# Performance work log

Measured on AMD Instinct MI355X. Metric: run time of the kernel, lower is better.

The kernel has to match this reference:

```python
import jax, jax.numpy as jnp
import numpy as np

MAX_ITER = 20
F_TOL = 1e-6
FREE_NUM = 64  # free_idx[1] + 1
TRUNC = (0, 512)  # truncate_idx


def setup_inputs() -> dict:
    key = jax.random.key(0)
    ks = jax.random.split(key, 8)
    bsz, in_dim, hid, out_dim, m = 1024, 512, 1024, 256, 128
    return {
        "b_primal": jax.random.normal(ks[0], (bsz, in_dim), jnp.float32),
        "W0": jax.random.normal(ks[1], (hid, in_dim), jnp.float32) / np.sqrt(in_dim).astype(np.float32),
        "b0": jnp.zeros((hid,), jnp.float32),
        "W1": jax.random.normal(ks[2], (hid, hid), jnp.float32) / np.sqrt(hid).astype(np.float32),
        "b1": jnp.zeros((hid,), jnp.float32),
        "W2": jax.random.normal(ks[3], (out_dim, hid), jnp.float32) / np.sqrt(hid).astype(np.float32),
        "b2": jnp.zeros((out_dim,), jnp.float32),
        "A": jax.random.normal(ks[4], (m, out_dim), jnp.float32) * 0.1,
        "b_vec": jax.random.normal(ks[5], (m,), jnp.float32),
        # scaled so spectral norm < 1 -> contracting fixed-point iteration
        "WzProj": jax.random.normal(ks[6], (out_dim, out_dim), jnp.float32) * 0.03,
        "WbProj": jax.random.normal(ks[7], (out_dim, m), jnp.float32) * 0.1,
    }


def reference(b_primal, W0, b0, W1, b1, W2, b2, A, b_vec, WzProj, WbProj):
    # eval-mode forward of DualNN (report_projection=True)
    x = b_primal[:, TRUNC[0]:TRUNC[1]]
    h = jax.nn.relu(x @ W0.T + b0)
    h = jax.nn.relu(h @ W1.T + b1)
    out = h @ W2.T + b2                      # [bsz, output_dim]

    bias_proj = b_vec @ WbProj.T             # [output_dim]

    def cond(state):
        _, it, res = state
        return (it <= MAX_ITER) & (res > F_TOL)

    def body(state):
        z, it, _ = state
        z = bias_proj + z @ WzProj.T         # affine projection step
        u = z[:, :FREE_NUM]
        v = jax.nn.relu(z[:, FREE_NUM:])     # clamp non-free coordinates
        z = jnp.concatenate([u, v], axis=-1)
        res = jnp.max(jnp.abs(z @ A.T - b_vec))  # inf-norm equality residual
        return z, it + 1, res

    z_star, curr_iter, _ = jax.lax.while_loop(
        cond, body, (out, jnp.int32(1), jnp.float32(jnp.inf)))
    return (z_star, out, curr_iter)
```

## Files before the change

kernel.cpp:

```cpp
#include <hip/hip_runtime.h>

typedef __attribute__((ext_vector_type(8))) __bf16 bf16x8;
typedef __attribute__((ext_vector_type(4))) float f32x4;

#define MAX_ITER_N 20
#define F_TOL_F 1e-6f
#define FREE_NUM_N 64

#define BSZ 1024
#define IN_DIM 512
#define HID 1024
#define OUT_DIM 256
#define M_CON 128

#define WS_BP    0
#define WS_RES   256
#define WS_CTRL  288
#define WS_H1    296
#define WS_H2    (WS_H1 + 524288)
#define WS_APC   (WS_H2 + 524288)
#define WS_W0C   (WS_APC + 262144)
#define WS_W1C   (WS_W0C + 262144)
#define WS_W2C   (WS_W1C + 524288)
#define WS_WZG   (WS_W2C + 131072)
#define WS_AG    (WS_WZG + 32768)

__device__ __forceinline__ unsigned short f2bf(float f) {
    unsigned int u = __float_as_uint(f);
    u += 0x7fffu + ((u >> 16) & 1u);
    return (unsigned short)(u >> 16);
}

__device__ __forceinline__ void gload_lds16(const unsigned short* g, unsigned short* l) {
    __builtin_amdgcn_global_load_lds(
        (const __attribute__((address_space(1))) unsigned int*)(const void*)g,
        (__attribute__((address_space(3))) unsigned int*)(void*)l, 16, 0, 0);
}

__global__ __launch_bounds__(256) void prep_k(
    const float* __restrict__ b_primal, const float* __restrict__ W0,
    const float* __restrict__ W1, const float* __restrict__ W2,
    const float* __restrict__ Wz, const float* __restrict__ Am,
    const float* __restrict__ b_vec, const float* __restrict__ WbProj,
    unsigned short* __restrict__ APc, unsigned short* __restrict__ W0c,
    unsigned short* __restrict__ W1c, unsigned short* __restrict__ W2c,
    unsigned short* __restrict__ WzG, unsigned short* __restrict__ AG,
    float* __restrict__ bp, unsigned int* __restrict__ res)
{
    int b = blockIdx.x;
    if (b >= 2400) {
        int j = threadIdx.x;
        float s = 0.0f;
        for (int k = 0; k < M_CON; ++k) s += b_vec[k] * WbProj[j * M_CON + k];
        bp[j] = s;
        if (j < 32) res[j] = 0u;
        return;
    }
    const float* src; unsigned short* dst; int off;
    if (b < 512)       { src = b_primal; dst = APc; off = b; }
    else if (b < 1024) { src = W0; dst = W0c; off = b - 512; }
    else if (b < 2048) { src = W1; dst = W1c; off = b - 1024; }
    else if (b < 2304) { src = W2; dst = W2c; off = b - 2048; }
    else if (b < 2368) { src = Wz; dst = WzG; off = b - 2304; }
    else               { src = Am; dst = AG;  off = b - 2368; }
    int idx = off * 1024 + threadIdx.x * 4;
    float4 v = *(const float4*)(src + idx);
    ushort4 o;
    o.x = f2bf(v.x); o.y = f2bf(v.y); o.z = f2bf(v.z); o.w = f2bf(v.w);
    *(ushort4*)(dst + idx) = o;
}

__device__ __forceinline__ void stage_tile(const unsigned short* __restrict__ src,
                                           unsigned short* lds, int ldK, int w, int lane) {
#pragma unroll
    for (int i = 0; i < 2; ++i) {
        int gbase = i * 256 + w * 64;
        int g = gbase + lane;
        int row = g >> 3;
        int sgc = (g & 7) ^ (row & 7);
        gload_lds16(src + row * ldK + sgc * 8, lds + gbase * 8);
    }
}

__device__ __forceinline__ bf16x8 frag_ld(const unsigned short* lds, int row, int j) {
    int phys = j ^ (row & 7);
    return __builtin_bit_cast(bf16x8, *(const uint4*)(lds + row * 64 + phys * 8));
}

template<int K, bool RELU, bool F32OUT>
__global__ __launch_bounds__(256) void mfma_gemm(
    const unsigned short* __restrict__ A,
    const unsigned short* __restrict__ B,
    const float* __restrict__ bias,
    void* __restrict__ Cv, int N_)
{
    __shared__ __align__(16) unsigned short As[64 * 64];
    __shared__ __align__(16) unsigned short Bs[64 * 64];
    const int tid = threadIdx.x;
    const int w = tid >> 6;
    const int lane = tid & 63;
    const int ln = lane & 15;
    const int q  = lane >> 4;
    const int row0 = blockIdx.y * 64;
    const int col0 = blockIdx.x * 64;

    const unsigned short* Ab = A + row0 * K;
    const unsigned short* Bb = B + col0 * K;

    f32x4 acc[2][2];
#pragma unroll
    for (int rt = 0; rt < 2; ++rt)
#pragma unroll
        for (int ct = 0; ct < 2; ++ct)
            acc[rt][ct] = (f32x4){0.f, 0.f, 0.f, 0.f};

    for (int k0 = 0; k0 < K; k0 += 64) {
        stage_tile(Ab + k0, As, K, w, lane);
        stage_tile(Bb + k0, Bs, K, w, lane);
        __syncthreads();
#pragma unroll
        for (int ks = 0; ks < 2; ++ks) {
            bf16x8 af[2], bfv[2];
#pragma unroll
            for (int rt = 0; rt < 2; ++rt)
                af[rt] = frag_ld(As, (w >> 1) * 32 + rt * 16 + ln, ks * 4 + q);
#pragma unroll
            for (int ct = 0; ct < 2; ++ct)
                bfv[ct] = frag_ld(Bs, (w & 1) * 32 + ct * 16 + ln, ks * 4 + q);
#pragma unroll
            for (int rt = 0; rt < 2; ++rt)
#pragma unroll
                for (int ct = 0; ct < 2; ++ct)
                    acc[rt][ct] = __builtin_amdgcn_mfma_f32_16x16x32_bf16(
                        af[rt], bfv[ct], acc[rt][ct], 0, 0, 0);
        }
        __syncthreads();
    }

    float bv[2];
#pragma unroll
    for (int ct = 0; ct < 2; ++ct)
        bv[ct] = bias[col0 + (w & 1) * 32 + ct * 16 + ln];
#pragma unroll
    for (int rt = 0; rt < 2; ++rt)
#pragma unroll
        for (int ct = 0; ct < 2; ++ct) {
            int c = col0 + (w & 1) * 32 + ct * 16 + ln;
#pragma unroll
            for (int i = 0; i < 4; ++i) {
                int r = row0 + (w >> 1) * 32 + rt * 16 + q * 4 + i;
                float v = acc[rt][ct][i] + bv[ct];
                if (RELU) v = fmaxf(v, 0.0f);
                if (F32OUT) ((float*)Cv)[r * N_ + c] = v;
                else ((unsigned short*)Cv)[r * N_ + c] = f2bf(v);
            }
        }
}

__global__ __launch_bounds__(256, 1) void loop_fused_k(
    const float* __restrict__ z0,
    const unsigned short* __restrict__ WzG,
    const unsigned short* __restrict__ AG,
    const float* __restrict__ bp,
    const float* __restrict__ b_vec,
    float* __restrict__ zout_g,
    unsigned int* __restrict__ res)
{
    __shared__ unsigned short zS[16][264];
    __shared__ float red[4];

    const int tid  = threadIdx.x;
    const int wave = tid >> 6;
    const int lane = tid & 63;
    const int ln   = lane & 15;
    const int q    = lane >> 4;
    const int r0   = blockIdx.x * 16;

    {
        int row = tid >> 4;
        int c0  = (tid & 15) * 16;
        const float* src = z0 + (r0 + row) * OUT_DIM + c0;
#pragma unroll
        for (int i = 0; i < 16; ++i) zS[row][c0 + i] = f2bf(src[i]);
    }

    bf16x8 afr[2][8];
    float bvv[2];
#pragma unroll
    for (int mt = 0; mt < 2; ++mt) {
        int m = wave * 32 + mt * 16 + ln;
        bvv[mt] = b_vec[m];
#pragma unroll
        for (int ks = 0; ks < 8; ++ks)
            afr[mt][ks] = __builtin_bit_cast(bf16x8, *(const uint4*)(AG + m * OUT_DIM + ks * 32 + q * 8));
    }
    int colg[4];
    float bpv[4];
    bf16x8 wzfr[4][8];
#pragma unroll
    for (int nt = 0; nt < 4; ++nt) {
        colg[nt] = wave * 64 + nt * 16 + ln;
        bpv[nt]  = bp[colg[nt]];
#pragma unroll
        for (int ks = 0; ks < 8; ++ks)
            wzfr[nt][ks] = __builtin_bit_cast(bf16x8, *(const uint4*)(WzG + colg[nt] * OUT_DIM + ks * 32 + q * 8));
    }

    __syncthreads();

    bf16x8 zfr[8];
#pragma unroll
    for (int ks = 0; ks < 8; ++ks)
        zfr[ks] = __builtin_bit_cast(bf16x8, *(const uint4*)&zS[ln][ks * 32 + q * 8]);

    const f32x4 zero4 = {0.f, 0.f, 0.f, 0.f};

    for (int t = 1; t <= MAX_ITER_N; ++t) {
        f32x4 acc[4];
#pragma unroll
        for (int nt = 0; nt < 4; ++nt) acc[nt] = zero4;
#pragma unroll
        for (int ks = 0; ks < 8; ++ks)
#pragma unroll
            for (int nt = 0; nt < 4; ++nt)
                acc[nt] = __builtin_amdgcn_mfma_f32_16x16x32_bf16(zfr[ks], wzfr[nt][ks], acc[nt], 0, 0, 0);
        float vals[4][4];
#pragma unroll
        for (int nt = 0; nt < 4; ++nt)
#pragma unroll
            for (int i = 0; i < 4; ++i) {
                float v = acc[nt][i] + bpv[nt];
                if (colg[nt] >= FREE_NUM_N) v = fmaxf(v, 0.0f);
                vals[nt][i] = v;
            }
        if (t == MAX_ITER_N) {
#pragma unroll
            for (int nt = 0; nt < 4; ++nt)
#pragma unroll
                for (int i = 0; i < 4; ++i)
                    zout_g[(r0 + q * 4 + i) * OUT_DIM + colg[nt]] = vals[nt][i];
        }
        __syncthreads();
#pragma unroll
        for (int nt = 0; nt < 4; ++nt)
#pragma unroll
            for (int i = 0; i < 4; ++i)
                zS[q * 4 + i][colg[nt]] = f2bf(vals[nt][i]);
        __syncthreads();
#pragma unroll
        for (int ks = 0; ks < 8; ++ks)
            zfr[ks] = __builtin_bit_cast(bf16x8, *(const uint4*)&zS[ln][ks * 32 + q * 8]);

        f32x4 acc2[2];
        acc2[0] = zero4; acc2[1] = zero4;
#pragma unroll
        for (int ks = 0; ks < 8; ++ks)
#pragma unroll
            for (int mt = 0; mt < 2; ++mt)
                acc2[mt] = __builtin_amdgcn_mfma_f32_16x16x32_bf16(zfr[ks], afr[mt][ks], acc2[mt], 0, 0, 0);
        float lmax = 0.0f;
#pragma unroll
        for (int mt = 0; mt < 2; ++mt)
#pragma unroll
            for (int i = 0; i < 4; ++i)
                lmax = fmaxf(lmax, fabsf(acc2[mt][i] - bvv[mt]));
#pragma unroll
        for (int off = 32; off > 0; off >>= 1)
            lmax = fmaxf(lmax, __shfl_xor(lmax, off));
        if (lane == 0) red[wave] = lmax;
        __syncthreads();
        if (tid == 0) {
            float bm = fmaxf(fmaxf(red[0], red[1]), fmaxf(red[2], red[3]));
            atomicMax(res + (t - 1), __float_as_uint(bm));
        }
    }
}

__global__ void decide_k(const unsigned int* __restrict__ res, int* __restrict__ ctrl,
                         float* __restrict__ out) {
    int T = MAX_ITER_N;
    for (int t = 0; t < MAX_ITER_N; ++t) {
        float r = __uint_as_float(res[t]);
        if (!(r > F_TOL_F)) { T = t + 1; break; }
    }
    ctrl[0] = T;
    out[2 * BSZ * OUT_DIM] = (float)(T + 1);
}

__global__ __launch_bounds__(256) void fallback_k(
    const float* __restrict__ z0, const float* __restrict__ Wz,
    const float* __restrict__ bp, const int* __restrict__ ctrl,
    float* __restrict__ out)
{
    const int T = ctrl[0];
    if (T >= MAX_ITER_N) return;
    __shared__ float zS[16][257];
    const int r0 = blockIdx.x * 16;
    const int tid = threadIdx.x;
    const int row = tid >> 4;
    const int c0 = (tid & 15) * 16;
    for (int i = 0; i < 16; ++i) zS[row][c0 + i] = z0[(r0 + row) * OUT_DIM + c0 + i];
    __syncthreads();
    const int j = tid;
    const float bj = bp[j];
    for (int t = 0; t < T; ++t) {
        float acc[16] = {};
        for (int k = 0; k < OUT_DIM; ++k) {
            float w = Wz[j * OUT_DIM + k];
#pragma unroll
            for (int r = 0; r < 16; ++r) acc[r] += zS[r][k] * w;
        }
        __syncthreads();
#pragma unroll
        for (int r = 0; r < 16; ++r) {
            float v = acc[r] + bj;
            if (j >= FREE_NUM_N) v = fmaxf(v, 0.0f);
            zS[r][j] = v;
        }
        __syncthreads();
    }
    for (int i = 0; i < 16; ++i) out[(r0 + row) * OUT_DIM + c0 + i] = zS[row][c0 + i];
}

extern "C" void kernel_launch(void* const* d_in, const int* in_sizes, int n_in,
                              void* d_out, int out_size, void* d_ws, size_t ws_size,
                              hipStream_t stream) {
    const float* b_primal = (const float*)d_in[0];
    const float* W0     = (const float*)d_in[1];
    const float* b0     = (const float*)d_in[2];
    const float* W1     = (const float*)d_in[3];
    const float* b1     = (const float*)d_in[4];
    const float* W2     = (const float*)d_in[5];
    const float* b2     = (const float*)d_in[6];
    const float* Amat   = (const float*)d_in[7];
    const float* b_vec  = (const float*)d_in[8];
    const float* WzProj = (const float*)d_in[9];
    const float* WbProj = (const float*)d_in[10];
    float* out = (float*)d_out;
    float* ws  = (float*)d_ws;

    float* bp = ws + WS_BP;
    unsigned int* res = (unsigned int*)(ws + WS_RES);
    int* ctrl = (int*)(ws + WS_CTRL);
    unsigned short* h1c = (unsigned short*)(ws + WS_H1);
    unsigned short* h2c = (unsigned short*)(ws + WS_H2);
    unsigned short* APc = (unsigned short*)(ws + WS_APC);
    unsigned short* W0c = (unsigned short*)(ws + WS_W0C);
    unsigned short* W1c = (unsigned short*)(ws + WS_W1C);
    unsigned short* W2c = (unsigned short*)(ws + WS_W2C);
    unsigned short* WzG = (unsigned short*)(ws + WS_WZG);
    unsigned short* AG  = (unsigned short*)(ws + WS_AG);

    float* outz = out + BSZ * OUT_DIM;

    hipLaunchKernelGGL(prep_k, dim3(2401), dim3(256), 0, stream,
                       b_primal, W0, W1, W2, WzProj, Amat, b_vec, WbProj,
                       APc, W0c, W1c, W2c, WzG, AG, bp, res);

    hipLaunchKernelGGL((mfma_gemm<IN_DIM, true, false>), dim3(HID / 64, BSZ / 64), dim3(256),
                       0, stream, APc, W0c, b0, (void*)h1c, HID);
    hipLaunchKernelGGL((mfma_gemm<HID, true, false>), dim3(HID / 64, BSZ / 64), dim3(256),
                       0, stream, h1c, W1c, b1, (void*)h2c, HID);
    hipLaunchKernelGGL((mfma_gemm<HID, false, true>), dim3(OUT_DIM / 64, BSZ / 64), dim3(256),
                       0, stream, h2c, W2c, b2, (void*)outz, OUT_DIM);

    hipLaunchKernelGGL(loop_fused_k, dim3(BSZ / 16), dim3(256), 0, stream,
                       outz, WzG, AG, bp, b_vec, out, res);
    hipLaunchKernelGGL(decide_k, dim3(1), dim3(1), 0, stream, res, ctrl, out);
    hipLaunchKernelGGL(fallback_k, dim3(BSZ / 16), dim3(256), 0, stream,
                       outz, WzProj, bp, ctrl, out);
}
```

Before: 148.1 us.

## Fuse all stages into one persistent kernel with software grid barriers

Replaces the seven-kernel pipeline (prep, three GEMMs, fixed-point loop, decide, fallback) with a single persistent kernel of 256 blocks that separates phases with an atomic-counter grid barrier. A memset clears the barrier and residual slots before launch. The goal is to remove launch gaps and inter-kernel tail effects. In exchange, each GEMM is capped at one tile per block with 256 blocks and launch_bounds(256,1), the loop phase uses only 64 blocks, and correctness relies on all 256 blocks being co-resident.

```diff
diff --git a/kernel.cpp b/kernel.cpp
--- a/kernel.cpp
+++ b/kernel.cpp
@@ -12,11 +12,12 @@
 #define HID 1024
 #define OUT_DIM 256
 #define M_CON 128
-
-#define WS_BP    0
-#define WS_RES   256
-#define WS_CTRL  288
-#define WS_H1    296
+#define NBLK 256
+
+#define WS_BAR   0
+#define WS_RES   8
+#define WS_BP    48
+#define WS_H1    304
 #define WS_H2    (WS_H1 + 524288)
 #define WS_APC   (WS_H2 + 524288)
 #define WS_W0C   (WS_APC + 262144)
@@ -37,37 +38,20 @@
         (__attribute__((address_space(3))) unsigned int*)(void*)l, 16, 0, 0);
 }
 
-__global__ __launch_bounds__(256) void prep_k(
-    const float* __restrict__ b_primal, const float* __restrict__ W0,
-    const float* __restrict__ W1, const float* __restrict__ W2,
-    const float* __restrict__ Wz, const float* __restrict__ Am,
-    const float* __restrict__ b_vec, const float* __restrict__ WbProj,
-    unsigned short* __restrict__ APc, unsigned short* __restrict__ W0c,
-    unsigned short* __restrict__ W1c, unsigned short* __restrict__ W2c,
-    unsigned short* __restrict__ WzG, unsigned short* __restrict__ AG,
-    float* __restrict__ bp, unsigned int* __restrict__ res)
-{
-    int b = blockIdx.x;
-    if (b >= 2400) {
-        int j = threadIdx.x;
-        float s = 0.0f;
-        for (int k = 0; k < M_CON; ++k) s += b_vec[k] * WbProj[j * M_CON + k];
-        bp[j] = s;
-        if (j < 32) res[j] = 0u;
-        return;
-    }
-    const float* src; unsigned short* dst; int off;
-    if (b < 512)       { src = b_primal; dst = APc; off = b; }
-    else if (b < 1024) { src = W0; dst = W0c; off = b - 512; }
-    else if (b < 2048) { src = W1; dst = W1c; off = b - 1024; }
-    else if (b < 2304) { src = W2; dst = W2c; off = b - 2048; }
-    else if (b < 2368) { src = Wz; dst = WzG; off = b - 2304; }
-    else               { src = Am; dst = AG;  off = b - 2368; }
-    int idx = off * 1024 + threadIdx.x * 4;
-    float4 v = *(const float4*)(src + idx);
-    ushort4 o;
-    o.x = f2bf(v.x); o.y = f2bf(v.y); o.z = f2bf(v.z); o.w = f2bf(v.w);
-    *(ushort4*)(dst + idx) = o;
+__device__ __forceinline__ void grid_barrier(unsigned int* bar) {
+    __syncthreads();
+    if (threadIdx.x == 0) {
+        unsigned int g = __hip_atomic_load(&bar[1], __ATOMIC_RELAXED, __HIP_MEMORY_SCOPE_AGENT);
+        unsigned int a = __hip_atomic_fetch_add(&bar[0], 1u, __ATOMIC_ACQ_REL, __HIP_MEMORY_SCOPE_AGENT);
+        if (a == (unsigned int)(NBLK - 1)) {
+            __hip_atomic_store(&bar[0], 0u, __ATOMIC_RELAXED, __HIP_MEMORY_SCOPE_AGENT);
+            __hip_atomic_store(&bar[1], g + 1u, __ATOMIC_RELEASE, __HIP_MEMORY_SCOPE_AGENT);
+        } else {
+            while (__hip_atomic_load(&bar[1], __ATOMIC_ACQUIRE, __HIP_MEMORY_SCOPE_AGENT) == g)
+                __builtin_amdgcn_s_sleep(2);
+        }
+    }
+    __syncthreads();
 }
 
 __device__ __forceinline__ void stage_tile(const unsigned short* __restrict__ src,
@@ -87,23 +71,22 @@
     return __builtin_bit_cast(bf16x8, *(const uint4*)(lds + row * 64 + phys * 8));
 }
 
-template<int K, bool RELU, bool F32OUT>
-__global__ __launch_bounds__(256) void mfma_gemm(
-    const unsigned short* __restrict__ A,
-    const unsigned short* __restrict__ B,
-    const float* __restrict__ bias,
-    void* __restrict__ Cv, int N_)
+template<bool RELU, bool F32OUT>
+__device__ void gemm_dev(const unsigned short* __restrict__ A,
+                         const unsigned short* __restrict__ B,
+                         const float* __restrict__ bias, void* __restrict__ Cv,
+                         int N_, int K, int tilesN, int ntiles,
+                         unsigned short* As, unsigned short* Bs)
 {
-    __shared__ __align__(16) unsigned short As[64 * 64];
-    __shared__ __align__(16) unsigned short Bs[64 * 64];
+    const int tile = blockIdx.x;
+    if (tile >= ntiles) return;
     const int tid = threadIdx.x;
     const int w = tid >> 6;
     const int lane = tid & 63;
     const int ln = lane & 15;
     const int q  = lane >> 4;
-    const int row0 = blockIdx.y * 64;
-    const int col0 = blockIdx.x * 64;
-
+    const int row0 = (tile / tilesN) * 64;
+    const int col0 = (tile % tilesN) * 64;
     const unsigned short* Ab = A + row0 * K;
     const unsigned short* Bb = B + col0 * K;
 
@@ -157,169 +140,208 @@
         }
 }
 
-__global__ __launch_bounds__(256, 1) void loop_fused_k(
-    const float* __restrict__ z0,
-    const unsigned short* __restrict__ WzG,
-    const unsigned short* __restrict__ AG,
-    const float* __restrict__ bp,
-    const float* __restrict__ b_vec,
-    float* __restrict__ zout_g,
-    unsigned int* __restrict__ res)
+__global__ __launch_bounds__(256, 1) void mega_k(
+    const float* __restrict__ b_primal, const float* __restrict__ W0,
+    const float* __restrict__ b0, const float* __restrict__ W1,
+    const float* __restrict__ b1, const float* __restrict__ W2,
+    const float* __restrict__ b2, const float* __restrict__ Amat,
+    const float* __restrict__ b_vec, const float* __restrict__ WzProj,
+    const float* __restrict__ WbProj, float* __restrict__ out,
+    float* __restrict__ ws)
 {
-    __shared__ unsigned short zS[16][264];
-    __shared__ float red[4];
-
-    const int tid  = threadIdx.x;
-    const int wave = tid >> 6;
-    const int lane = tid & 63;
-    const int ln   = lane & 15;
-    const int q    = lane >> 4;
-    const int r0   = blockIdx.x * 16;
-
-    {
-        int row = tid >> 4;
-        int c0  = (tid & 15) * 16;
-        const float* src = z0 + (r0 + row) * OUT_DIM + c0;
-#pragma unroll
-        for (int i = 0; i < 16; ++i) zS[row][c0 + i] = f2bf(src[i]);
-    }
-
-    bf16x8 afr[2][8];
-    float bvv[2];
-#pragma unroll
-    for (int mt = 0; mt < 2; ++mt) {
-        int m = wave * 32 + mt * 16 + ln;
-        bvv[mt] = b_vec[m];
-#pragma unroll
-        for (int ks = 0; ks < 8; ++ks)
-            afr[mt][ks] = __builtin_bit_cast(bf16x8, *(const uint4*)(AG + m * OUT_DIM + ks * 32 + q * 8));
-    }
-    int colg[4];
-    float bpv[4];
-    bf16x8 wzfr[4][8];
-#pragma unroll
-    for (int nt = 0; nt < 4; ++nt) {
-        colg[nt] = wave * 64 + nt * 16 + ln;
-        bpv[nt]  = bp[colg[nt]];
-#pragma unroll
-        for (int ks = 0; ks < 8; ++ks)
-            wzfr[nt][ks] = __builtin_bit_cast(bf16x8, *(const uint4*)(WzG + colg[nt] * OUT_DIM + ks * 32 + q * 8));
-    }
-
-    __syncthreads();
-
-    bf16x8 zfr[8];
-#pragma unroll
-    for (int ks = 0; ks < 8; ++ks)
-        zfr[ks] = __builtin_bit_cast(bf16x8, *(const uint4*)&zS[ln][ks * 32 + q * 8]);
-
-    const f32x4 zero4 = {0.f, 0.f, 0.f, 0.f};
-
-    for (int t = 1; t <= MAX_ITER_N; ++t) {
-        f32x4 acc[4];
-#pragma unroll
-        for (int nt = 0; nt < 4; ++nt) acc[nt] = zero4;
-#pragma unroll
-        for (int ks = 0; ks < 8; ++ks)
-#pragma unroll
-            for (int nt = 0; nt < 4; ++nt)
-                acc[nt] = __builtin_amdgcn_mfma_f32_16x16x32_bf16(zfr[ks], wzfr[nt][ks], acc[nt], 0, 0, 0);
-        float vals[4][4];
-#pragma unroll
-        for (int nt = 0; nt < 4; ++nt)
-#pragma unroll
-            for (int i = 0; i < 4; ++i) {
-                float v = acc[nt][i] + bpv[nt];
-                if (colg[nt] >= FREE_NUM_N) v = fmaxf(v, 0.0f);
-                vals[nt][i] = v;
-            }
-        if (t == MAX_ITER_N) {
-#pragma unroll
-            for (int nt = 0; nt < 4; ++nt)
-#pragma unroll
-                for (int i = 0; i < 4; ++i)
-                    zout_g[(r0 + q * 4 + i) * OUT_DIM + colg[nt]] = vals[nt][i];
+    __shared__ __align__(16) unsigned char smem[64 * 64 * 2 * 2 + 256];
+    unsigned short* As = (unsigned short*)smem;
+    unsigned short* Bs = As + 64 * 64;
+
+    unsigned int* bar = (unsigned int*)(ws + WS_BAR);
+    unsigned int* res = (unsigned int*)(ws + WS_RES);
+    float* bp = ws + WS_BP;
+    unsigned short* h1c = (unsigned short*)(ws + WS_H1);
+    unsigned short* h2c = (unsigned short*)(ws + WS_H2);
+    unsigned short* APc = (unsigned short*)(ws + WS_APC);
+    unsigned short* W0c = (unsigned short*)(ws + WS_W0C);
+    unsigned short* W1c = (unsigned short*)(ws + WS_W1C);
+    unsigned short* W2c = (unsigned short*)(ws + WS_W2C);
+    unsigned short* WzG = (unsigned short*)(ws + WS_WZG);
+    unsigned short* AG  = (unsigned short*)(ws + WS_AG);
+    float* outz = out + BSZ * OUT_DIM;
+
+    const int tid = threadIdx.x;
+
+    for (int u = blockIdx.x; u <= 2400; u += NBLK) {
+        if (u == 2400) {
+            float s = 0.0f;
+            for (int k = 0; k < M_CON; ++k) s += b_vec[k] * WbProj[tid * M_CON + k];
+            bp[tid] = s;
+            continue;
+        }
+        const float* src; unsigned short* dst; int off;
+        if (u < 512)       { src = b_primal; dst = APc; off = u; }
+        else if (u < 1024) { src = W0; dst = W0c; off = u - 512; }
+        else if (u < 2048) { src = W1; dst = W1c; off = u - 1024; }
+        else if (u < 2304) { src = W2; dst = W2c; off = u - 2048; }
+        else if (u < 2368) { src = WzProj; dst = WzG; off = u - 2304; }
+        else               { src = Amat; dst = AG;  off = u - 2368; }
+        int idx = off * 1024 + tid * 4;
+        float4 v = *(const float4*)(src + idx);
+        ushort4 o;
+        o.x = f2bf(v.x); o.y = f2bf(v.y); o.z = f2bf(v.z); o.w = f2bf(v.w);
+        *(ushort4*)(dst + idx) = o;
+    }
+    grid_barrier(bar);
+
+    gemm_dev<true, false>(APc, W0c, b0, (void*)h1c, HID, IN_DIM, 16, 256, As, Bs);
+    grid_barrier(bar);
+    gemm_dev<true, false>(h1c, W1c, b1, (void*)h2c, HID, HID, 16, 256, As, Bs);
+    grid_barrier(bar);
+    gemm_dev<false, true>(h2c, W2c, b2, (void*)outz, OUT_DIM, HID, 4, 64, As, Bs);
+    grid_barrier(bar);
+
+    if (blockIdx.x < 64) {
+        unsigned short (*zS)[264] = (unsigned short(*)[264])smem;
+        float* red = (float*)(smem + 16 * 264 * 2);
+
+        const int wave = tid >> 6;
+        const int lane = tid & 63;
+        const int ln   = lane & 15;
+        const int q    = lane >> 4;
+        const int r0   = blockIdx.x * 16;
+
+        {
+            int row = tid >> 4;
+            int c0  = (tid & 15) * 16;
+            const float* src = outz + (r0 + row) * OUT_DIM + c0;
+#pragma unroll
+            for (int i = 0; i < 16; ++i) zS[row][c0 + i] = f2bf(src[i]);
+        }
+
+        bf16x8 afr[2][8];
+        float bvv[2];
+#pragma unroll
+        for (int mt = 0; mt < 2; ++mt) {
+            int m = wave * 32 + mt * 16 + ln;
+            bvv[mt] = b_vec[m];
+#pragma unroll
+            for (int ks = 0; ks < 8; ++ks)
+                afr[mt][ks] = __builtin_bit_cast(bf16x8, *(const uint4*)(AG + m * OUT_DIM + ks * 32 + q * 8));
+        }
+        int colg[4];
+        float bpv[4];
+        bf16x8 wzfr[4][8];
+#pragma unroll
+        for (int nt = 0; nt < 4; ++nt) {
+            colg[nt] = wave * 64 + nt * 16 + ln;
+            bpv[nt]  = bp[colg[nt]];
+#pragma unroll
+            for (int ks = 0; ks < 8; ++ks)
+                wzfr[nt][ks] = __builtin_bit_cast(bf16x8, *(const uint4*)(WzG + colg[nt] * OUT_DIM + ks * 32 + q * 8));
         }
         __syncthreads();
-#pragma unroll
-        for (int nt = 0; nt < 4; ++nt)
-#pragma unroll
-            for (int i = 0; i < 4; ++i)
-                zS[q * 4 + i][colg[nt]] = f2bf(vals[nt][i]);
-        __syncthreads();
+
+        bf16x8 zfr[8];
 #pragma unroll
         for (int ks = 0; ks < 8; ++ks)
             zfr[ks] = __builtin_bit_cast(bf16x8, *(const uint4*)&zS[ln][ks * 32 + q * 8]);
 
-        f32x4 acc2[2];
-        acc2[0] = zero4; acc2[1] = zero4;
-#pragma unroll
-        for (int ks = 0; ks < 8; ++ks)
+        const f32x4 zero4 = {0.f, 0.f, 0.f, 0.f};
+
+        for (int t = 1; t <= MAX_ITER_N; ++t) {
+            f32x4 acc[4];
+#pragma unroll
+            for (int nt = 0; nt < 4; ++nt) acc[nt] = zero4;
+#pragma unroll
+            for (int ks = 0; ks < 8; ++ks)
+#pragma unroll
+                for (int nt = 0; nt < 4; ++nt)
+                    acc[nt] = __builtin_amdgcn_mfma_f32_16x16x32_bf16(zfr[ks], wzfr[nt][ks], acc[nt], 0, 0, 0);
+            float vals[4][4];
+#pragma unroll
+            for (int nt = 0; nt < 4; ++nt)
+#pragma unroll
+                for (int i = 0; i < 4; ++i) {
+                    float v = acc[nt][i] + bpv[nt];
+                    if (colg[nt] >= FREE_NUM_N) v = fmaxf(v, 0.0f);
+                    vals[nt][i] = v;
+                }
+            if (t == MAX_ITER_N) {
+#pragma unroll
+                for (int nt = 0; nt < 4; ++nt)
+#pragma unroll
+                    for (int i = 0; i < 4; ++i)
+                        out[(r0 + q * 4 + i) * OUT_DIM + colg[nt]] = vals[nt][i];
+            }
+            __syncthreads();
+#pragma unroll
+            for (int nt = 0; nt < 4; ++nt)
+#pragma unroll
+                for (int i = 0; i < 4; ++i)
+                    zS[q * 4 + i][colg[nt]] = f2bf(vals[nt][i]);
+            __syncthreads();
+#pragma unroll
+            for (int ks = 0; ks < 8; ++ks)
+                zfr[ks] = __builtin_bit_cast(bf16x8, *(const uint4*)&zS[ln][ks * 32 + q * 8]);
+
+            f32x4 acc2[2];
+            acc2[0] = zero4; acc2[1] = zero4;
+#pragma unroll
+            for (int ks = 0; ks < 8; ++ks)
+#pragma unroll
+                for (int mt = 0; mt < 2; ++mt)
+                    acc2[mt] = __builtin_amdgcn_mfma_f32_16x16x32_bf16(zfr[ks], afr[mt][ks], acc2[mt], 0, 0, 0);
+            float lmax = 0.0f;
 #pragma unroll
             for (int mt = 0; mt < 2; ++mt)
-                acc2[mt] = __builtin_amdgcn_mfma_f32_16x16x32_bf16(zfr[ks], afr[mt][ks], acc2[mt], 0, 0, 0);
-        float lmax = 0.0f;
-#pragma unroll
-        for (int mt = 0; mt < 2; ++mt)
-#pragma unroll
-            for (int i = 0; i < 4; ++i)
-                lmax = fmaxf(lmax, fabsf(acc2[mt][i] - bvv[mt]));
-#pragma unroll
-        for (int off = 32; off > 0; off >>= 1)
-            lmax = fmaxf(lmax, __shfl_xor(lmax, off));
-        if (lane == 0) red[wave] = lmax;
-        __syncthreads();
-        if (tid == 0) {
-            float bm = fmaxf(fmaxf(red[0], red[1]), fmaxf(red[2], red[3]));
-            atomicMax(res + (t - 1), __float_as_uint(bm));
-        }
-    }
-}
-
-__global__ void decide_k(const unsigned int* __restrict__ res, int* __restrict__ ctrl,
-                         float* __restrict__ out) {
+#pragma unroll
+                for (int i = 0; i < 4; ++i)
+                    lmax = fmaxf(lmax, fabsf(acc2[mt][i] - bvv[mt]));
+#pragma unroll
+            for (int off = 32; off > 0; off >>= 1)
+                lmax = fmaxf(lmax, __shfl_xor(lmax, off));
+            if (lane == 0) red[wave] = lmax;
+            __syncthreads();
+            if (tid == 0) {
+                float bm = fmaxf(fmaxf(red[0], red[1]), fmaxf(red[2], red[3]));
+                atomicMax(res + (t - 1), __float_as_uint(bm));
+            }
+        }
+    }
+    grid_barrier(bar);
+
     int T = MAX_ITER_N;
     for (int t = 0; t < MAX_ITER_N; ++t) {
         float r = __uint_as_float(res[t]);
         if (!(r > F_TOL_F)) { T = t + 1; break; }
     }
-    ctrl[0] = T;
-    out[2 * BSZ * OUT_DIM] = (float)(T + 1);
-}
-
-__global__ __launch_bounds__(256) void fallback_k(
-    const float* __restrict__ z0, const float* __restrict__ Wz,
-    const float* __restrict__ bp, const int* __restrict__ ctrl,
-    float* __restrict__ out)
-{
-    const int T = ctrl[0];
-    if (T >= MAX_ITER_N) return;
-    __shared__ float zS[16][257];
-    const int r0 = blockIdx.x * 16;
-    const int tid = threadIdx.x;
-    const int row = tid >> 4;
-    const int c0 = (tid & 15) * 16;
-    for (int i = 0; i < 16; ++i) zS[row][c0 + i] = z0[(r0 + row) * OUT_DIM + c0 + i];
-    __syncthreads();
-    const int j = tid;
-    const float bj = bp[j];
-    for (int t = 0; t < T; ++t) {
-        float acc[16] = {};
-        for (int k = 0; k < OUT_DIM; ++k) {
-            float w = Wz[j * OUT_DIM + k];
-#pragma unroll
-            for (int r = 0; r < 16; ++r) acc[r] += zS[r][k] * w;
-        }
+    if (blockIdx.x == 0 && tid == 0)
+        out[2 * BSZ * OUT_DIM] = (float)(T + 1);
+
+    if (T < MAX_ITER_N && blockIdx.x < 64) {
+        float (*zF)[257] = (float(*)[257])smem;
+        const int r0 = blockIdx.x * 16;
+        const int row = tid >> 4;
+        const int c0 = (tid & 15) * 16;
+        for (int i = 0; i < 16; ++i) zF[row][c0 + i] = outz[(r0 + row) * OUT_DIM + c0 + i];
         __syncthreads();
-#pragma unroll
-        for (int r = 0; r < 16; ++r) {
-            float v = acc[r] + bj;
-            if (j >= FREE_NUM_N) v = fmaxf(v, 0.0f);
-            zS[r][j] = v;
-        }
-        __syncthreads();
-    }
-    for (int i = 0; i < 16; ++i) out[(r0 + row) * OUT_DIM + c0 + i] = zS[row][c0 + i];
+        const int j = tid;
+        const float bj = bp[j];
+        for (int t = 0; t < T; ++t) {
+            float acc[16] = {};
+            for (int k = 0; k < OUT_DIM; ++k) {
+                float w = WzProj[j * OUT_DIM + k];
+#pragma unroll
+                for (int r = 0; r < 16; ++r) acc[r] += zF[r][k] * w;
+            }
+            __syncthreads();
+#pragma unroll
+            for (int r = 0; r < 16; ++r) {
+                float v = acc[r] + bj;
+                if (j >= FREE_NUM_N) v = fmaxf(v, 0.0f);
+                zF[r][j] = v;
+            }
+            __syncthreads();
+        }
+        for (int i = 0; i < 16; ++i) out[(r0 + row) * OUT_DIM + c0 + i] = zF[row][c0 + i];
+    }
 }
 
 extern "C" void kernel_launch(void* const* d_in, const int* in_sizes, int n_in,
@@ -339,34 +361,9 @@
     float* out = (float*)d_out;
     float* ws  = (float*)d_ws;
 
-    float* bp = ws + WS_BP;
-    unsigned int* res = (unsigned int*)(ws + WS_RES);
-    int* ctrl = (int*)(ws + WS_CTRL);
-    unsigned short* h1c = (unsigned short*)(ws + WS_H1);
-    unsigned short* h2c = (unsigned short*)(ws + WS_H2);
-    unsigned short* APc = (unsigned short*)(ws + WS_APC);
-    unsigned short* W0c = (unsigned short*)(ws + WS_W0C);
-    unsigned short* W1c = (unsigned short*)(ws + WS_W1C);
-    unsigned short* W2c = (unsigned short*)(ws + WS_W2C);
-    unsigned short* WzG = (unsigned short*)(ws + WS_WZG);
-    unsigned short* AG  = (unsigned short*)(ws + WS_AG);
-
-    float* outz = out + BSZ * OUT_DIM;
-
-    hipLaunchKernelGGL(prep_k, dim3(2401), dim3(256), 0, stream,
-                       b_primal, W0, W1, W2, WzProj, Amat, b_vec, WbProj,
-                       APc, W0c, W1c, W2c, WzG, AG, bp, res);
-
-    hipLaunchKernelGGL((mfma_gemm<IN_DIM, true, false>), dim3(HID / 64, BSZ / 64), dim3(256),
-                       0, stream, APc, W0c, b0, (void*)h1c, HID);
-    hipLaunchKernelGGL((mfma_gemm<HID, true, false>), dim3(HID / 64, BSZ / 64), dim3(256),
-                       0, stream, h1c, W1c, b1, (void*)h2c, HID);
-    hipLaunchKernelGGL((mfma_gemm<HID, false, true>), dim3(OUT_DIM / 64, BSZ / 64), dim3(256),
-                       0, stream, h2c, W2c, b2, (void*)outz, OUT_DIM);
-
-    hipLaunchKernelGGL(loop_fused_k, dim3(BSZ / 16), dim3(256), 0, stream,
-                       outz, WzG, AG, bp, b_vec, out, res);
-    hipLaunchKernelGGL(decide_k, dim3(1), dim3(1), 0, stream, res, ctrl, out);
-    hipLaunchKernelGGL(fallback_k, dim3(BSZ / 16), dim3(256), 0, stream,
-                       outz, WzProj, bp, ctrl, out);
-}
+    hipMemsetAsync(ws, 0, (WS_BP) * sizeof(float), stream);
+
+    hipLaunchKernelGGL(mega_k, dim3(NBLK), dim3(256), 0, stream,
+                       b_primal, W0, b0, W1, b1, W2, b2, Amat, b_vec,
+                       WzProj, WbProj, out, ws);
+}
```

After: 323.3 us. 118% more time.
